# Kernel optimization log

Measured on AMD Instinct MI355X. Metric: run time of the kernel, lower is better.

Reference implementation:

```python
import jax, jax.numpy as jnp
import numpy as np

N = 50000
E = 800000
F_IN = 128
F_HID = 128
F_OUT = 64


def setup_inputs() -> dict:
    key = jax.random.key(0)
    ks = jax.random.split(key, 16)
    x = jax.random.normal(ks[0], (N, F_IN), dtype=jnp.float32)
    ei1 = jax.random.randint(ks[1], (2, E), 0, N, dtype=jnp.int32)
    ei2 = jax.random.randint(ks[2], (2, E), 0, N, dtype=jnp.int32)
    ei3 = jax.random.randint(ks[3], (2, E), 0, N, dtype=jnp.int32)
    s = lambda k, i, o: jax.random.normal(k, (i, o), dtype=jnp.float32) / np.sqrt(i)
    Wl1 = s(ks[4], F_IN, F_HID); Wr1 = s(ks[5], F_IN, F_HID); b1 = jnp.zeros((F_HID,), jnp.float32)
    Wl2 = s(ks[6], F_HID, F_HID); Wr2 = s(ks[7], F_HID, F_HID); b2 = jnp.zeros((F_HID,), jnp.float32)
    Wl3 = s(ks[8], F_HID, F_OUT); Wr3 = s(ks[9], F_HID, F_OUT); b3 = jnp.zeros((F_OUT,), jnp.float32)
    return {"x": x, "ei1": ei1, "ei2": ei2, "ei3": ei3,
            "Wl1": Wl1, "Wr1": Wr1, "b1": b1,
            "Wl2": Wl2, "Wr2": Wr2, "b2": b2,
            "Wl3": Wl3, "Wr3": Wr3, "b3": b3}


def sage_conv(x, ei, Wl, Wr, b):
    # mean aggregation over incoming edges: src=ei[0] -> dst=ei[1]
    msg = x[ei[0]]                                            # [E, F]
    agg = jax.ops.segment_sum(msg, ei[1], num_segments=N)     # [N, F]
    cnt = jax.ops.segment_sum(jnp.ones((ei.shape[1],), x.dtype), ei[1], num_segments=N)
    mean = agg / jnp.maximum(cnt, 1.0)[:, None]
    # out = lin_l(mean) + lin_r(x_target); full-graph so x_target = x
    return mean @ Wl + b + x @ Wr


def reference(x, ei1, ei2, ei3, Wl1, Wr1, b1, Wl2, Wr2, b2, Wl3, Wr3, b3):
    # in_conv + relu (dropout is identity in eval mode)
    h = jax.nn.relu(sage_conv(x, ei1, Wl1, Wr1, b1))
    # mid_conv + relu + residual skip
    m = jax.nn.relu(sage_conv(h, ei2, Wl2, Wr2, b2))
    h = m + h
    # out_conv (no norm, no activation)
    return sage_conv(h, ei3, Wl3, Wr3, b3)
```

## Files before the change

### kernel.cpp

```cpp
#include <hip/hip_runtime.h>

#define FDIM 128
#define NBMAX 128
#define CAPB 10240

typedef short short8 __attribute__((ext_vector_type(8)));
typedef float f32x4 __attribute__((ext_vector_type(4)));

static __device__ __forceinline__ unsigned short f2bf(float f) {
    unsigned u = __float_as_uint(f);
    u += 0x7FFF + ((u >> 16) & 1);
    return (unsigned short)(u >> 16);
}
static __device__ __forceinline__ float bf2f(unsigned short h) {
    return __uint_as_float(((unsigned)h) << 16);
}

__global__ __launch_bounds__(256) void pack_kernel(
    int* __restrict__ gCnt, int nb3,
    const float* __restrict__ Wl1, const float* __restrict__ Wr1,
    const float* __restrict__ Wl2, const float* __restrict__ Wr2,
    const float* __restrict__ Wl3, const float* __restrict__ Wr3,
    ushort* __restrict__ Wp1, ushort* __restrict__ Wp2, ushort* __restrict__ Wp3)
{
    int b = blockIdx.x;
    if (b == 0) {
        for (int k = threadIdx.x; k < nb3; k += 256) gCnt[k] = 0;
    }
    if (b < 32) {
        const float *Wl, *Wr; ushort* Wp; int base;
        if (b < 16) { Wl = Wl1; Wr = Wr1; Wp = Wp1; base = b; }
        else        { Wl = Wl2; Wr = Wr2; Wp = Wp2; base = b - 16; }
        int idx = base * 256 + threadIdx.x;
        int lane = idx & 63;
        int jt = (idx >> 6) % 8;
        int kt = (idx >> 6) / 8;
        int kbase = kt * 32 + (lane >> 4) * 8;
        int j = jt * 16 + (lane & 15);
        const float* W = (kbase < 128) ? Wl : Wr;
        int kb = kbase & 127;
        ushort tmp[8];
#pragma unroll
        for (int t = 0; t < 8; ++t) tmp[t] = f2bf(W[(size_t)(kb + t) * 128 + j]);
        *reinterpret_cast<uint4*>(Wp + (size_t)idx * 8) = *reinterpret_cast<uint4*>(tmp);
        return;
    }
    int idx = (b - 32) * 256 + threadIdx.x;
    if (idx >= 4 * 8 * 64) return;
    int lane = idx & 63;
    int jt = (idx >> 6) % 8;
    int kt = (idx >> 6) / 8;
    int kbase = kt * 32 + (lane >> 4) * 8;
    int j = jt * 16 + (lane & 15);
    const float* W = (j < 64) ? Wl3 : Wr3;
    int jj = j & 63;
    ushort tmp[8];
#pragma unroll
    for (int t = 0; t < 8; ++t) tmp[t] = f2bf(W[(size_t)(kbase + t) * 64 + jj]);
    *reinterpret_cast<uint4*>(Wp3 + (size_t)idx * 8) = *reinterpret_cast<uint4*>(tmp);
}

__global__ __launch_bounds__(256) void binconv_kernel(
    const int* __restrict__ ei1, const int* __restrict__ ei2, const int* __restrict__ ei3,
    int* __restrict__ gCnt, unsigned* __restrict__ binned,
    int E, int NB, int bpg,
    const float* __restrict__ x, ushort* __restrict__ xb, int n4)
{
    __shared__ int hist[NBMAX];
    __shared__ int excl[NBMAX];
    __shared__ int cursor[NBMAX];
    __shared__ int gbase[NBMAX];
    __shared__ unsigned stag[4096];

    const int nbin = 3 * bpg;
    if ((int)blockIdx.x >= nbin) {
        int i = (blockIdx.x - nbin) * 256 + threadIdx.x;
        if (i >= n4) return;
        float4 v = reinterpret_cast<const float4*>(x)[i];
        ushort4 o = { f2bf(v.x), f2bf(v.y), f2bf(v.z), f2bf(v.w) };
        reinterpret_cast<ushort4*>(xb)[i] = o;
        return;
    }
    const int g = blockIdx.x / bpg;
    const int c = blockIdx.x % bpg;
    const int* ei = (g == 0) ? ei1 : (g == 1) ? ei2 : ei3;
    const int e0 = c * 4096;
    const int chunk = min(4096, E - e0);
    const int t = threadIdx.x;

    if (t < NB) hist[t] = 0;
    __syncthreads();
    for (int i = t; i < chunk; i += 256)
        atomicAdd(&hist[ei[E + e0 + i] >> 9], 1);
    __syncthreads();
    if (t < 64) {
        int a = (2 * t     < NB) ? hist[2 * t]     : 0;
        int b = (2 * t + 1 < NB) ? hist[2 * t + 1] : 0;
        int s = a + b, incl = s;
#pragma unroll
        for (int d = 1; d < 64; d <<= 1) {
            int x2 = __shfl_up(incl, d);
            if (t >= d) incl += x2;
        }
        int ex = incl - s;
        if (2 * t     < NB) { excl[2 * t]     = ex;     cursor[2 * t]     = ex; }
        if (2 * t + 1 < NB) { excl[2 * t + 1] = ex + a; cursor[2 * t + 1] = ex + a; }
    }
    __syncthreads();
    if (t < NB) {
        int cnt = hist[t];
        gbase[t] = cnt ? atomicAdd(&gCnt[g * NB + t], cnt) : 0;
    }
    __syncthreads();
    for (int i = t; i < chunk; i += 256) {
        int src = ei[e0 + i];
        int dst = ei[E + e0 + i];
        int pl = atomicAdd(&cursor[dst >> 9], 1);
        stag[pl] = ((unsigned)dst << 16) | (unsigned)src;
    }
    __syncthreads();
    for (int i = t; i < chunk; i += 256) {
        unsigned u = stag[i];
        int bk = u >> 25;
        int off = gbase[bk] + (i - excl[bk]);
        if (off < CAPB)
            binned[(size_t)(g * NB + bk) * CAPB + off] = u;
    }
}

__global__ __launch_bounds__(256) void fill2_kernel(
    const unsigned* __restrict__ binned, const int* __restrict__ gCnt,
    int* __restrict__ rowptr, ushort* __restrict__ colu, int N, int NB)
{
    __shared__ int hist[512];
    __shared__ int cursor[512];
    __shared__ int wsum[4];
    __shared__ int sColBase, sTotal;

    const int M = 3 * NB;
    const int gb = blockIdx.x;
    const int g = gb / NB, b = gb % NB;
    const int t = threadIdx.x;
    const int lane = t & 63, w = t >> 6;

    {
        int v0 = (2 * t     < M) ? gCnt[2 * t]     : 0;
        int v1 = (2 * t + 1 < M) ? gCnt[2 * t + 1] : 0;
        int s2 = v0 + v1, incl = s2;
#pragma unroll
        for (int d = 1; d < 64; d <<= 1) {
            int x = __shfl_up(incl, d);
            if (lane >= d) incl += x;
        }
        if (lane == 63) wsum[w] = incl;
        __syncthreads();
        int woff = 0;
        for (int ww = 0; ww < w; ++ww) woff += wsum[ww];
        int ex = woff + incl - s2;
        if (2 * t     == gb) sColBase = ex;
        if (2 * t + 1 == gb) sColBase = ex + v0;
        if (2 * t     == M - 1) sTotal = ex + v0;
        if (2 * t + 1 == M - 1) sTotal = ex + v0 + v1;
        __syncthreads();
    }
    const int colBase = sColBase;
    if (gb == 0 && t == 0) rowptr[(size_t)3 * N] = sTotal;

    const int n0 = b << 9;
    const int NL = min(512, N - n0);
    const int cnt = min(gCnt[gb], CAPB);
    const size_t ebase = (size_t)gb * CAPB;

    __syncthreads();
    hist[t] = 0; hist[t + 256] = 0;
    __syncthreads();
    for (int e = t; e < cnt; e += 256)
        atomicAdd(&hist[(binned[ebase + e] >> 16) & 511], 1);
    __syncthreads();
    int a = hist[2 * t], bb = hist[2 * t + 1];
    int s2 = a + bb, incl = s2;
#pragma unroll
    for (int d = 1; d < 64; d <<= 1) {
        int x = __shfl_up(incl, d);
        if (lane >= d) incl += x;
    }
    if (lane == 63) wsum[w] = incl;
    __syncthreads();
    int woff = 0;
    for (int ww = 0; ww < w; ++ww) woff += wsum[ww];
    int ex = woff + incl - s2;
    if (2 * t     < NL) rowptr[(size_t)g * N + n0 + 2 * t]     = colBase + ex;
    if (2 * t + 1 < NL) rowptr[(size_t)g * N + n0 + 2 * t + 1] = colBase + ex + a;
    cursor[2 * t] = ex; cursor[2 * t + 1] = ex + a;
    __syncthreads();
    for (int e = t; e < cnt; e += 256) {
        unsigned u = binned[ebase + e];
        int pl = atomicAdd(&cursor[(u >> 16) & 511], 1);
        colu[colBase + pl] = (ushort)(u & 0xFFFFu);
    }
}

static __device__ __forceinline__ float4 unpk_lo(uint4 v) {
    return make_float4(__uint_as_float(v.x << 16), __uint_as_float(v.x & 0xFFFF0000u),
                       __uint_as_float(v.y << 16), __uint_as_float(v.y & 0xFFFF0000u));
}
static __device__ __forceinline__ float4 unpk_hi(uint4 v) {
    return make_float4(__uint_as_float(v.z << 16), __uint_as_float(v.z & 0xFFFF0000u),
                       __uint_as_float(v.w << 16), __uint_as_float(v.w & 0xFFFF0000u));
}

static __device__ __forceinline__ uint4 gather_mean(
    const ushort* __restrict__ src, const int* __restrict__ rp,
    const ushort* __restrict__ col, int n, int l)
{
    int beg = rp[n], end = rp[n + 1];
    float4 a0 = make_float4(0.f, 0.f, 0.f, 0.f);
    float4 a1 = make_float4(0.f, 0.f, 0.f, 0.f);
    int e = beg;
    for (; e + 8 <= end; e += 8) {
        uint4 v0 = *reinterpret_cast<const uint4*>(src + ((size_t)col[e]     << 7) + l * 8);
        uint4 v1 = *reinterpret_cast<const uint4*>(src + ((size_t)col[e + 1] << 7) + l * 8);
        uint4 v2 = *reinterpret_cast<const uint4*>(src + ((size_t)col[e + 2] << 7) + l * 8);
        uint4 v3 = *reinterpret_cast<const uint4*>(src + ((size_t)col[e + 3] << 7) + l * 8);
        uint4 v4 = *reinterpret_cast<const uint4*>(src + ((size_t)col[e + 4] << 7) + l * 8);
        uint4 v5 = *reinterpret_cast<const uint4*>(src + ((size_t)col[e + 5] << 7) + l * 8);
        uint4 v6 = *reinterpret_cast<const uint4*>(src + ((size_t)col[e + 6] << 7) + l * 8);
        uint4 v7 = *reinterpret_cast<const uint4*>(src + ((size_t)col[e + 7] << 7) + l * 8);
        a0 += unpk_lo(v0); a1 += unpk_hi(v0);
        a0 += unpk_lo(v1); a1 += unpk_hi(v1);
        a0 += unpk_lo(v2); a1 += unpk_hi(v2);
        a0 += unpk_lo(v3); a1 += unpk_hi(v3);
        a0 += unpk_lo(v4); a1 += unpk_hi(v4);
        a0 += unpk_lo(v5); a1 += unpk_hi(v5);
        a0 += unpk_lo(v6); a1 += unpk_hi(v6);
        a0 += unpk_lo(v7); a1 += unpk_hi(v7);
    }
    if (e < end) {
        int last = end - 1;
        int c0 = col[e];
        int c1 = col[min(e + 1, last)];
        int c2 = col[min(e + 2, last)];
        int c3 = col[min(e + 3, last)];
        int c4 = col[min(e + 4, last)];
        int c5 = col[min(e + 5, last)];
        int c6 = col[min(e + 6, last)];
        int c7 = col[min(e + 7, last)];
        uint4 v0 = *reinterpret_cast<const uint4*>(src + ((size_t)c0 << 7) + l * 8);
        uint4 v1 = *reinterpret_cast<const uint4*>(src + ((size_t)c1 << 7) + l * 8);
        uint4 v2 = *reinterpret_cast<const uint4*>(src + ((size_t)c2 << 7) + l * 8);
        uint4 v3 = *reinterpret_cast<const uint4*>(src + ((size_t)c3 << 7) + l * 8);
        uint4 v4 = *reinterpret_cast<const uint4*>(src + ((size_t)c4 << 7) + l * 8);
        uint4 v5 = *reinterpret_cast<const uint4*>(src + ((size_t)c5 << 7) + l * 8);
        uint4 v6 = *reinterpret_cast<const uint4*>(src + ((size_t)c6 << 7) + l * 8);
        uint4 v7 = *reinterpret_cast<const uint4*>(src + ((size_t)c7 << 7) + l * 8);
        float m1 = (e + 1 <= last) ? 1.f : 0.f;
        float m2 = (e + 2 <= last) ? 1.f : 0.f;
        float m3 = (e + 3 <= last) ? 1.f : 0.f;
        float m4 = (e + 4 <= last) ? 1.f : 0.f;
        float m5 = (e + 5 <= last) ? 1.f : 0.f;
        float m6 = (e + 6 <= last) ? 1.f : 0.f;
        float m7 = (e + 7 <= last) ? 1.f : 0.f;
        a0 += unpk_lo(v0);      a1 += unpk_hi(v0);
        a0 += unpk_lo(v1) * m1; a1 += unpk_hi(v1) * m1;
        a0 += unpk_lo(v2) * m2; a1 += unpk_hi(v2) * m2;
        a0 += unpk_lo(v3) * m3; a1 += unpk_hi(v3) * m3;
        a0 += unpk_lo(v4) * m4; a1 += unpk_hi(v4) * m4;
        a0 += unpk_lo(v5) * m5; a1 += unpk_hi(v5) * m5;
        a0 += unpk_lo(v6) * m6; a1 += unpk_hi(v6) * m6;
        a0 += unpk_lo(v7) * m7; a1 += unpk_hi(v7) * m7;
    }
    int deg = end - beg;
    float inv = 1.0f / (float)(deg > 1 ? deg : 1);
    uint4 o;
    o.x = (unsigned)f2bf(a0.x * inv) | ((unsigned)f2bf(a0.y * inv) << 16);
    o.y = (unsigned)f2bf(a0.z * inv) | ((unsigned)f2bf(a0.w * inv) << 16);
    o.z = (unsigned)f2bf(a1.x * inv) | ((unsigned)f2bf(a1.y * inv) << 16);
    o.w = (unsigned)f2bf(a1.z * inv) | ((unsigned)f2bf(a1.w * inv) << 16);
    return o;
}

__global__ __launch_bounds__(256) void fused_l1(
    const ushort* __restrict__ xb, const int* __restrict__ rp,
    const ushort* __restrict__ col, const ushort* __restrict__ Wp,
    const float* __restrict__ bias, ushort* __restrict__ hb, int N)
{
    __shared__ __align__(16) ushort sA[16 * 256];
    const int tid = threadIdx.x;
    const int grp = tid >> 4;
    const int l = tid & 15;
    const int n0 = blockIdx.x * 16;
    int n = n0 + grp; if (n >= N) n = N - 1;

    {
        uint4 v = *reinterpret_cast<const uint4*>(xb + ((size_t)n << 7) + l * 8);
        int s = 16 + l;
        int sp = (s & 24) | ((s ^ grp) & 7);
        *reinterpret_cast<uint4*>(&sA[(grp << 8) + (sp << 3)]) = v;
    }
    {
        uint4 o = gather_mean(xb, rp, col, n, l);
        int sp = (l & 24) | ((l ^ grp) & 7);
        *reinterpret_cast<uint4*>(&sA[(grp << 8) + (sp << 3)]) = o;
    }
    __syncthreads();

    const int lane = tid & 63;
    const int w = tid >> 6;
    const int rloc = lane & 15;
    const int q = lane >> 4;

    f32x4 acc[2];
    acc[0] = (f32x4){0.f, 0.f, 0.f, 0.f};
    acc[1] = (f32x4){0.f, 0.f, 0.f, 0.f};
#pragma unroll
    for (int kt = 0; kt < 8; ++kt) {
        int s = kt * 4 + q;
        int sp = (s & 24) | ((s ^ rloc) & 7);
        short8 a = *reinterpret_cast<const short8*>(&sA[(rloc << 8) + (sp << 3)]);
#pragma unroll
        for (int jj = 0; jj < 2; ++jj) {
            int jt = w * 2 + jj;
            short8 b = *reinterpret_cast<const short8*>(Wp + ((size_t)((kt * 8 + jt) * 64 + lane) << 3));
            acc[jj] = __builtin_amdgcn_mfma_f32_16x16x32_bf16(a, b, acc[jj], 0, 0, 0);
        }
    }

#pragma unroll
    for (int jj = 0; jj < 2; ++jj) {
        int j = (w * 2 + jj) * 16 + (lane & 15);
        float bj = bias[j];
#pragma unroll
        for (int reg = 0; reg < 4; ++reg) {
            int nn = n0 + q * 4 + reg;
            if (nn < N)
                hb[((size_t)nn << 7) + j] = f2bf(fmaxf(acc[jj][reg] + bj, 0.f));
        }
    }
}

__global__ __launch_bounds__(256) void fused_l23(
    const ushort* __restrict__ hb, const int* __restrict__ rp,
    const ushort* __restrict__ col,
    const ushort* __restrict__ Wp2, const float* __restrict__ b2,
    const ushort* __restrict__ Wp3, const float* __restrict__ b3,
    ushort* __restrict__ y3, float* __restrict__ out, int N)
{
    __shared__ __align__(16) ushort sA[16 * 256];
    __shared__ __align__(16) ushort sH[16 * 128];
    const int tid = threadIdx.x;
    const int grp = tid >> 4;
    const int l = tid & 15;
    const int n0 = blockIdx.x * 16;
    int n = n0 + grp; if (n >= N) n = N - 1;

    {
        uint4 v = *reinterpret_cast<const uint4*>(hb + ((size_t)n << 7) + l * 8);
        int s = 16 + l;
        int sp = (s & 24) | ((s ^ grp) & 7);
        *reinterpret_cast<uint4*>(&sA[(grp << 8) + (sp << 3)]) = v;
    }
    {
        uint4 o = gather_mean(hb, rp, col, n, l);
        int sp = (l & 24) | ((l ^ grp) & 7);
        *reinterpret_cast<uint4*>(&sA[(grp << 8) + (sp << 3)]) = o;
    }
    __syncthreads();

    const int lane = tid & 63;
    const int w = tid >> 6;
    const int rloc = lane & 15;
    const int q = lane >> 4;

    f32x4 acc[2];
    acc[0] = (f32x4){0.f, 0.f, 0.f, 0.f};
    acc[1] = (f32x4){0.f, 0.f, 0.f, 0.f};
#pragma unroll
    for (int kt = 0; kt < 8; ++kt) {
        int s = kt * 4 + q;
        int sp = (s & 24) | ((s ^ rloc) & 7);
        short8 a = *reinterpret_cast<const short8*>(&sA[(rloc << 8) + (sp << 3)]);
#pragma unroll
        for (int jj = 0; jj < 2; ++jj) {
            int jt = w * 2 + jj;
            short8 b = *reinterpret_cast<const short8*>(Wp2 + ((size_t)((kt * 8 + jt) * 64 + lane) << 3));
            acc[jj] = __builtin_amdgcn_mfma_f32_16x16x32_bf16(a, b, acc[jj], 0, 0, 0);
        }
    }

#pragma unroll
    for (int jj = 0; jj < 2; ++jj) {
        int j = (w * 2 + jj) * 16 + (lane & 15);
        float bj = b2[j];
        int sSelf = 16 + (j >> 3);
        int s = j >> 3;
#pragma unroll
        for (int reg = 0; reg < 4; ++reg) {
            int r = q * 4 + reg;
            int spSelf = (sSelf & 24) | ((sSelf ^ r) & 7);
            float hself = bf2f(sA[(r << 8) + (spSelf << 3) + (j & 7)]);
            float v = fmaxf(acc[jj][reg] + bj, 0.f) + hself;
            int sp = (s & 8) | ((s ^ r) & 7);
            sH[(r << 7) + (sp << 3) + (j & 7)] = f2bf(v);
        }
    }
    __syncthreads();

    acc[0] = (f32x4){0.f, 0.f, 0.f, 0.f};
    acc[1] = (f32x4){0.f, 0.f, 0.f, 0.f};
#pragma unroll
    for (int kt = 0; kt < 4; ++kt) {
        int s = kt * 4 + q;
        int sp = (s & 8) | ((s ^ rloc) & 7);
        short8 a = *reinterpret_cast<const short8*>(&sH[(rloc << 7) + (sp << 3)]);
#pragma unroll
        for (int jj = 0; jj < 2; ++jj) {
            int jt = w * 2 + jj;
            short8 b = *reinterpret_cast<const short8*>(Wp3 + ((size_t)((kt * 8 + jt) * 64 + lane) << 3));
            acc[jj] = __builtin_amdgcn_mfma_f32_16x16x32_bf16(a, b, acc[jj], 0, 0, 0);
        }
    }

#pragma unroll
    for (int jj = 0; jj < 2; ++jj) {
        int jt = w * 2 + jj;
        int j = jt * 16 + (lane & 15);
#pragma unroll
        for (int reg = 0; reg < 4; ++reg) {
            int nn = n0 + q * 4 + reg;
            if (nn < N) {
                if (jt < 4) {
                    y3[((size_t)nn << 6) + j] = f2bf(acc[jj][reg]);
                } else {
                    out[((size_t)nn << 6) + (j - 64)] = acc[jj][reg] + b3[j - 64];
                }
            }
        }
    }
}

__global__ __launch_bounds__(256) void gather3_kernel(
    const ushort* __restrict__ y3, const int* __restrict__ rp,
    const ushort* __restrict__ col, float* __restrict__ out, int N)
{
    int node = blockIdx.x * 32 + (threadIdx.x >> 3);
    if (node >= N) return;
    int l = threadIdx.x & 7;
    int beg = rp[node], end = rp[node + 1];
    float4 a0 = make_float4(0.f, 0.f, 0.f, 0.f);
    float4 a1 = make_float4(0.f, 0.f, 0.f, 0.f);

    int e = beg;
    for (; e + 8 <= end; e += 8) {
        uint4 v0 = *reinterpret_cast<const uint4*>(y3 + ((size_t)col[e]     << 6) + l * 8);
        uint4 v1 = *reinterpret_cast<const uint4*>(y3 + ((size_t)col[e + 1] << 6) + l * 8);
        uint4 v2 = *reinterpret_cast<const uint4*>(y3 + ((size_t)col[e + 2] << 6) + l * 8);
        uint4 v3 = *reinterpret_cast<const uint4*>(y3 + ((size_t)col[e + 3] << 6) + l * 8);
        uint4 v4 = *reinterpret_cast<const uint4*>(y3 + ((size_t)col[e + 4] << 6) + l * 8);
        uint4 v5 = *reinterpret_cast<const uint4*>(y3 + ((size_t)col[e + 5] << 6) + l * 8);
        uint4 v6 = *reinterpret_cast<const uint4*>(y3 + ((size_t)col[e + 6] << 6) + l * 8);
        uint4 v7 = *reinterpret_cast<const uint4*>(y3 + ((size_t)col[e + 7] << 6) + l * 8);
        a0 += unpk_lo(v0); a1 += unpk_hi(v0);
        a0 += unpk_lo(v1); a1 += unpk_hi(v1);
        a0 += unpk_lo(v2); a1 += unpk_hi(v2);
        a0 += unpk_lo(v3); a1 += unpk_hi(v3);
        a0 += unpk_lo(v4); a1 += unpk_hi(v4);
        a0 += unpk_lo(v5); a1 += unpk_hi(v5);
        a0 += unpk_lo(v6); a1 += unpk_hi(v6);
        a0 += unpk_lo(v7); a1 += unpk_hi(v7);
    }
    if (e < end) {
        int last = end - 1;
        int c0 = col[e];
        int c1 = col[min(e + 1, last)];
        int c2 = col[min(e + 2, last)];
        int c3 = col[min(e + 3, last)];
        int c4 = col[min(e + 4, last)];
        int c5 = col[min(e + 5, last)];
        int c6 = col[min(e + 6, last)];
        int c7 = col[min(e + 7, last)];
        uint4 v0 = *reinterpret_cast<const uint4*>(y3 + ((size_t)c0 << 6) + l * 8);
        uint4 v1 = *reinterpret_cast<const uint4*>(y3 + ((size_t)c1 << 6) + l * 8);
        uint4 v2 = *reinterpret_cast<const uint4*>(y3 + ((size_t)c2 << 6) + l * 8);
        uint4 v3 = *reinterpret_cast<const uint4*>(y3 + ((size_t)c3 << 6) + l * 8);
        uint4 v4 = *reinterpret_cast<const uint4*>(y3 + ((size_t)c4 << 6) + l * 8);
        uint4 v5 = *reinterpret_cast<const uint4*>(y3 + ((size_t)c5 << 6) + l * 8);
        uint4 v6 = *reinterpret_cast<const uint4*>(y3 + ((size_t)c6 << 6) + l * 8);
        uint4 v7 = *reinterpret_cast<const uint4*>(y3 + ((size_t)c7 << 6) + l * 8);
        float m1 = (e + 1 <= last) ? 1.f : 0.f;
        float m2 = (e + 2 <= last) ? 1.f : 0.f;
        float m3 = (e + 3 <= last) ? 1.f : 0.f;
        float m4 = (e + 4 <= last) ? 1.f : 0.f;
        float m5 = (e + 5 <= last) ? 1.f : 0.f;
        float m6 = (e + 6 <= last) ? 1.f : 0.f;
        float m7 = (e + 7 <= last) ? 1.f : 0.f;
        a0 += unpk_lo(v0);      a1 += unpk_hi(v0);
        a0 += unpk_lo(v1) * m1; a1 += unpk_hi(v1) * m1;
        a0 += unpk_lo(v2) * m2; a1 += unpk_hi(v2) * m2;
        a0 += unpk_lo(v3) * m3; a1 += unpk_hi(v3) * m3;
        a0 += unpk_lo(v4) * m4; a1 += unpk_hi(v4) * m4;
        a0 += unpk_lo(v5) * m5; a1 += unpk_hi(v5) * m5;
        a0 += unpk_lo(v6) * m6; a1 += unpk_hi(v6) * m6;
        a0 += unpk_lo(v7) * m7; a1 += unpk_hi(v7) * m7;
    }

    int deg = end - beg;
    float inv = 1.0f / (float)(deg > 1 ? deg : 1);
    float* po = out + ((size_t)node << 6) + l * 8;
    float4 o0 = *reinterpret_cast<const float4*>(po);
    float4 o1 = *reinterpret_cast<const float4*>(po + 4);
    o0.x += a0.x * inv; o0.y += a0.y * inv; o0.z += a0.z * inv; o0.w += a0.w * inv;
    o1.x += a1.x * inv; o1.y += a1.y * inv; o1.z += a1.z * inv; o1.w += a1.w * inv;
    *reinterpret_cast<float4*>(po)     = o0;
    *reinterpret_cast<float4*>(po + 4) = o1;
}

extern "C" void kernel_launch(void* const* d_in, const int* in_sizes, int n_in,
                              void* d_out, int out_size, void* d_ws, size_t ws_size,
                              hipStream_t stream) {
    const float* x   = (const float*)d_in[0];
    const int*   ei1 = (const int*)d_in[1];
    const int*   ei2 = (const int*)d_in[2];
    const int*   ei3 = (const int*)d_in[3];
    const float* Wl1 = (const float*)d_in[4];
    const float* Wr1 = (const float*)d_in[5];
    const float* b1  = (const float*)d_in[6];
    const float* Wl2 = (const float*)d_in[7];
    const float* Wr2 = (const float*)d_in[8];
    const float* b2  = (const float*)d_in[9];
    const float* Wl3 = (const float*)d_in[10];
    const float* Wr3 = (const float*)d_in[11];
    const float* b3  = (const float*)d_in[12];
    float* out = (float*)d_out;

    const int N = in_sizes[0] / FDIM;
    const int E = in_sizes[1] / 2;
    const int NB = (N + 511) >> 9;

    auto al = [](size_t v) { return (v + 255) & ~(size_t)255; };
    char* ws = (char*)d_ws;
    ushort* xb   = (ushort*)ws;   ws += al((size_t)N * FDIM * 2);
    ushort* hb   = (ushort*)ws;   ws += al((size_t)N * FDIM * 2);
    ushort* y3   = (ushort*)ws;   ws += al((size_t)N * 64 * 2);
    ushort* Wp1  = (ushort*)ws;   ws += al((size_t)8 * 8 * 64 * 8 * 2);
    ushort* Wp2  = (ushort*)ws;   ws += al((size_t)8 * 8 * 64 * 8 * 2);
    ushort* Wp3  = (ushort*)ws;   ws += al((size_t)4 * 8 * 64 * 8 * 2);
    int*     rowptr = (int*)ws;   ws += al((size_t)(3 * N + 1) * 4);
    int*     gCnt   = (int*)ws;   ws += al((size_t)(3 * NB) * 4);
    unsigned* binned = (unsigned*)ws; ws += al((size_t)3 * NB * CAPB * 4);
    ushort*  colu   = (ushort*)ws;

    const int bpg = (E + 4095) / 4096;
    const int n4  = N * FDIM / 4;
    const int fusedBlocks   = (N + 15) / 16;
    const int gather3Blocks = (N + 31) / 32;

    pack_kernel<<<40, 256, 0, stream>>>(
        gCnt, 3 * NB, Wl1, Wr1, Wl2, Wr2, Wl3, Wr3, Wp1, Wp2, Wp3);

    binconv_kernel<<<3 * bpg + (n4 + 255) / 256, 256, 0, stream>>>(
        ei1, ei2, ei3, gCnt, binned, E, NB, bpg, x, xb, n4);

    fill2_kernel<<<3 * NB, 256, 0, stream>>>(binned, gCnt, rowptr, colu, N, NB);

    fused_l1<<<fusedBlocks, 256, 0, stream>>>(xb, rowptr, colu, Wp1, b1, hb, N);

    fused_l23<<<fusedBlocks, 256, 0, stream>>>(
        hb, rowptr + N, colu, Wp2, b2, Wp3, b3, y3, out, N);

    gather3_kernel<<<gather3Blocks, 256, 0, stream>>>(y3, rowptr + 2 * N, colu, out, N);
}
```

Measured before the change: 145.6 us.

## Process nodes in degree-sorted order to balance gather work per wavefront

Adds a per-graph degree histogram in fill2 and a new permsort kernel that builds a counting-sort permutation of nodes by in-degree (capped at 63). The fused layer kernels and the final gather then visit nodes through this permutation, so the 16 nodes sharing a block, and the 8-lane groups sharing a wavefront, have similar degrees and less divergence in the gather loop. The cost is an extra kernel launch, extra global atomics, an indirection load per node, and scattered output writes instead of contiguous ones.

After: 298.3 us. +104.9%, slower.

```diff
diff --git a/kernel.cpp b/kernel.cpp
--- a/kernel.cpp
+++ b/kernel.cpp
@@ -17,7 +17,7 @@
 }
 
 __global__ __launch_bounds__(256) void pack_kernel(
-    int* __restrict__ gCnt, int nb3,
+    int* __restrict__ gCnt, int nzero,
     const float* __restrict__ Wl1, const float* __restrict__ Wr1,
     const float* __restrict__ Wl2, const float* __restrict__ Wr2,
     const float* __restrict__ Wl3, const float* __restrict__ Wr3,
@@ -25,7 +25,7 @@
 {
     int b = blockIdx.x;
     if (b == 0) {
-        for (int k = threadIdx.x; k < nb3; k += 256) gCnt[k] = 0;
+        for (int k = threadIdx.x; k < nzero; k += 256) gCnt[k] = 0;
     }
     if (b < 32) {
         const float *Wl, *Wr; ushort* Wp; int base;
@@ -130,11 +130,13 @@
 
 __global__ __launch_bounds__(256) void fill2_kernel(
     const unsigned* __restrict__ binned, const int* __restrict__ gCnt,
-    int* __restrict__ rowptr, ushort* __restrict__ colu, int N, int NB)
+    int* __restrict__ rowptr, ushort* __restrict__ colu,
+    int* __restrict__ degHist, int N, int NB)
 {
     __shared__ int hist[512];
     __shared__ int cursor[512];
     __shared__ int wsum[4];
+    __shared__ int dh[64];
     __shared__ int sColBase, sTotal;
 
     const int M = 3 * NB;
@@ -173,6 +175,7 @@
 
     __syncthreads();
     hist[t] = 0; hist[t + 256] = 0;
+    if (t < 64) dh[t] = 0;
     __syncthreads();
     for (int e = t; e < cnt; e += 256)
         atomicAdd(&hist[(binned[ebase + e] >> 16) & 511], 1);
@@ -192,11 +195,43 @@
     if (2 * t     < NL) rowptr[(size_t)g * N + n0 + 2 * t]     = colBase + ex;
     if (2 * t + 1 < NL) rowptr[(size_t)g * N + n0 + 2 * t + 1] = colBase + ex + a;
     cursor[2 * t] = ex; cursor[2 * t + 1] = ex + a;
-    __syncthreads();
+    if (2 * t     < NL) atomicAdd(&dh[min(a, 63)], 1);
+    if (2 * t + 1 < NL) atomicAdd(&dh[min(bb, 63)], 1);
+    __syncthreads();
+    if (t < 64 && dh[t]) atomicAdd(&degHist[g * 64 + t], dh[t]);
     for (int e = t; e < cnt; e += 256) {
         unsigned u = binned[ebase + e];
         int pl = atomicAdd(&cursor[(u >> 16) & 511], 1);
         colu[colBase + pl] = (ushort)(u & 0xFFFFu);
+    }
+}
+
+__global__ __launch_bounds__(256) void permsort_kernel(
+    const int* __restrict__ rowptr, const int* __restrict__ degHist,
+    int* __restrict__ degCur, int* __restrict__ perm, int N, int npg)
+{
+    __shared__ int base[64];
+    const int g = blockIdx.x / npg;
+    const int c = blockIdx.x % npg;
+    const int t = threadIdx.x;
+    if (t < 64) {
+        int v = degHist[g * 64 + t];
+        int incl = v;
+#pragma unroll
+        for (int d = 1; d < 64; d <<= 1) {
+            int x = __shfl_up(incl, d);
+            if (t >= d) incl += x;
+        }
+        base[t] = incl - v;
+    }
+    __syncthreads();
+    int lo = c * 2048;
+    int hi = min(lo + 2048, N);
+    for (int i = lo + t; i < hi; i += 256) {
+        int d = rowptr[(size_t)g * N + i + 1] - rowptr[(size_t)g * N + i];
+        d = min(d, 63);
+        int pos = base[d] + atomicAdd(&degCur[g * 64 + d], 1);
+        perm[(size_t)g * N + pos] = i;
     }
 }
 
@@ -281,15 +316,19 @@
 
 __global__ __launch_bounds__(256) void fused_l1(
     const ushort* __restrict__ xb, const int* __restrict__ rp,
-    const ushort* __restrict__ col, const ushort* __restrict__ Wp,
-    const float* __restrict__ bias, ushort* __restrict__ hb, int N)
+    const ushort* __restrict__ col, const int* __restrict__ perm,
+    const ushort* __restrict__ Wp, const float* __restrict__ bias,
+    ushort* __restrict__ hb, int N)
 {
     __shared__ __align__(16) ushort sA[16 * 256];
+    __shared__ int sNode[16];
     const int tid = threadIdx.x;
     const int grp = tid >> 4;
     const int l = tid & 15;
     const int n0 = blockIdx.x * 16;
-    int n = n0 + grp; if (n >= N) n = N - 1;
+    int gidx = n0 + grp; if (gidx >= N) gidx = N - 1;
+    int n = perm[gidx];
+    if (l == 0) sNode[grp] = n;
 
     {
         uint4 v = *reinterpret_cast<const uint4*>(xb + ((size_t)n << 7) + l * 8);
@@ -331,27 +370,32 @@
         float bj = bias[j];
 #pragma unroll
         for (int reg = 0; reg < 4; ++reg) {
-            int nn = n0 + q * 4 + reg;
-            if (nn < N)
+            int gi = n0 + q * 4 + reg;
+            if (gi < N) {
+                int nn = sNode[q * 4 + reg];
                 hb[((size_t)nn << 7) + j] = f2bf(fmaxf(acc[jj][reg] + bj, 0.f));
+            }
         }
     }
 }
 
 __global__ __launch_bounds__(256) void fused_l23(
     const ushort* __restrict__ hb, const int* __restrict__ rp,
-    const ushort* __restrict__ col,
+    const ushort* __restrict__ col, const int* __restrict__ perm,
     const ushort* __restrict__ Wp2, const float* __restrict__ b2,
     const ushort* __restrict__ Wp3, const float* __restrict__ b3,
     ushort* __restrict__ y3, float* __restrict__ out, int N)
 {
     __shared__ __align__(16) ushort sA[16 * 256];
     __shared__ __align__(16) ushort sH[16 * 128];
+    __shared__ int sNode[16];
     const int tid = threadIdx.x;
     const int grp = tid >> 4;
     const int l = tid & 15;
     const int n0 = blockIdx.x * 16;
-    int n = n0 + grp; if (n >= N) n = N - 1;
+    int gidx = n0 + grp; if (gidx >= N) gidx = N - 1;
+    int n = perm[gidx];
+    if (l == 0) sNode[grp] = n;
 
     {
         uint4 v = *reinterpret_cast<const uint4*>(hb + ((size_t)n << 7) + l * 8);
@@ -426,8 +470,9 @@
         int j = jt * 16 + (lane & 15);
 #pragma unroll
         for (int reg = 0; reg < 4; ++reg) {
-            int nn = n0 + q * 4 + reg;
-            if (nn < N) {
+            int gi = n0 + q * 4 + reg;
+            if (gi < N) {
+                int nn = sNode[q * 4 + reg];
                 if (jt < 4) {
                     y3[((size_t)nn << 6) + j] = f2bf(acc[jj][reg]);
                 } else {
@@ -440,10 +485,12 @@
 
 __global__ __launch_bounds__(256) void gather3_kernel(
     const ushort* __restrict__ y3, const int* __restrict__ rp,
-    const ushort* __restrict__ col, float* __restrict__ out, int N)
-{
-    int node = blockIdx.x * 32 + (threadIdx.x >> 3);
-    if (node >= N) return;
+    const ushort* __restrict__ col, const int* __restrict__ perm,
+    float* __restrict__ out, int N)
+{
+    int idx = blockIdx.x * 32 + (threadIdx.x >> 3);
+    if (idx >= N) return;
+    int node = perm[idx];
     int l = threadIdx.x & 7;
     int beg = rp[node], end = rp[node + 1];
     float4 a0 = make_float4(0.f, 0.f, 0.f, 0.f);
@@ -545,27 +592,34 @@
     ushort* Wp2  = (ushort*)ws;   ws += al((size_t)8 * 8 * 64 * 8 * 2);
     ushort* Wp3  = (ushort*)ws;   ws += al((size_t)4 * 8 * 64 * 8 * 2);
     int*     rowptr = (int*)ws;   ws += al((size_t)(3 * N + 1) * 4);
-    int*     gCnt   = (int*)ws;   ws += al((size_t)(3 * NB) * 4);
+    int*     gCnt   = (int*)ws;   ws += al(((size_t)(3 * NB) + 384) * 4);
+    int*     degHist = gCnt + 3 * NB;
+    int*     degCur  = degHist + 192;
+    int*     perm   = (int*)ws;   ws += al((size_t)(3 * N) * 4);
     unsigned* binned = (unsigned*)ws; ws += al((size_t)3 * NB * CAPB * 4);
     ushort*  colu   = (ushort*)ws;
 
     const int bpg = (E + 4095) / 4096;
     const int n4  = N * FDIM / 4;
+    const int npg = (N + 2047) / 2048;
     const int fusedBlocks   = (N + 15) / 16;
     const int gather3Blocks = (N + 31) / 32;
 
     pack_kernel<<<40, 256, 0, stream>>>(
-        gCnt, 3 * NB, Wl1, Wr1, Wl2, Wr2, Wl3, Wr3, Wp1, Wp2, Wp3);
+        gCnt, 3 * NB + 384, Wl1, Wr1, Wl2, Wr2, Wl3, Wr3, Wp1, Wp2, Wp3);
 
     binconv_kernel<<<3 * bpg + (n4 + 255) / 256, 256, 0, stream>>>(
         ei1, ei2, ei3, gCnt, binned, E, NB, bpg, x, xb, n4);
 
-    fill2_kernel<<<3 * NB, 256, 0, stream>>>(binned, gCnt, rowptr, colu, N, NB);
-
-    fused_l1<<<fusedBlocks, 256, 0, stream>>>(xb, rowptr, colu, Wp1, b1, hb, N);
+    fill2_kernel<<<3 * NB, 256, 0, stream>>>(binned, gCnt, rowptr, colu, degHist, N, NB);
+
+    permsort_kernel<<<3 * npg, 256, 0, stream>>>(rowptr, degHist, degCur, perm, N, npg);
+
+    fused_l1<<<fusedBlocks, 256, 0, stream>>>(xb, rowptr, colu, perm, Wp1, b1, hb, N);
 
     fused_l23<<<fusedBlocks, 256, 0, stream>>>(
-        hb, rowptr + N, colu, Wp2, b2, Wp3, b3, y3, out, N);
-
-    gather3_kernel<<<gather3Blocks, 256, 0, stream>>>(y3, rowptr + 2 * N, colu, out, N);
-}
+        hb, rowptr + N, colu, perm + N, Wp2, b2, Wp3, b3, y3, out, N);
+
+    gather3_kernel<<<gather3Blocks, 256, 0, stream>>>(
+        y3, rowptr + 2 * N, colu, perm + 2 * N, out, N);
+}
```
